# Performance work log

Measured on AMD Instinct MI355X. Metric: run time of the kernel, lower is better.

The kernel has to match this reference:

```python
import jax, jax.numpy as jnp
import numpy as np

B, F, D, H = 256, 128, 512, 8
HD = D // H
SPARSITY = 0.5
KVAL = max(1, int(F * SPARSITY))  # 64


def setup_inputs() -> dict:
    key = jax.random.key(0)
    ks = jax.random.split(key, 12)
    s = 0.02
    x = jax.random.normal(ks[0], (B, F, D), dtype=jnp.float32)
    Wq = jax.random.normal(ks[1], (D, D), dtype=jnp.float32) * s
    bq = jnp.zeros((D,), jnp.float32)
    Wk = jax.random.normal(ks[2], (D, D), dtype=jnp.float32) * s
    bk = jnp.zeros((D,), jnp.float32)
    Wv = jax.random.normal(ks[3], (D, D), dtype=jnp.float32) * s
    bv = jnp.zeros((D,), jnp.float32)
    Wo = jax.random.normal(ks[4], (D, D), dtype=jnp.float32) * s
    bo = jnp.zeros((D,), jnp.float32)
    # correlation prior init: 0.5 * exp(-0.1 * |i-j|)
    idx = jnp.arange(F, dtype=jnp.float32)
    corr_prior = 0.5 * jnp.exp(-0.1 * jnp.abs(idx[:, None] - idx[None, :]))
    feat_imp = jnp.ones((F,), jnp.float32)
    # price_vol_detector: Linear(2D->D), SiLU, Linear(D->1), Sigmoid
    W1 = jax.random.normal(ks[5], (2 * D, D), dtype=jnp.float32) * s
    b1 = jnp.zeros((D,), jnp.float32)
    W2 = jax.random.normal(ks[6], (D, 1), dtype=jnp.float32) * s
    b2 = jnp.zeros((1,), jnp.float32)
    return {"x": x, "Wq": Wq, "bq": bq, "Wk": Wk, "bk": bk, "Wv": Wv, "bv": bv,
            "Wo": Wo, "bo": bo, "corr_prior": corr_prior, "feat_imp": feat_imp,
            "W1": W1, "b1": b1, "W2": W2, "b2": b2}


def reference(x, Wq, bq, Wk, bk, Wv, bv, Wo, bo, corr_prior, feat_imp, W1, b1, W2, b2):
    def split_heads(t):  # [B,F,D] -> [B,H,F,HD]
        return t.reshape(B, F, H, HD).transpose(0, 2, 1, 3)

    q = split_heads(x @ Wq + bq)
    k = split_heads(x @ Wk + bk)
    v = split_heads(x @ Wv + bv)

    scores = jnp.einsum('bhqd,bhkd->bhqk', q, k) / np.sqrt(HD).astype(np.float32)

    # correlation prior * pairwise feature importance
    imp = feat_imp[:, None] * feat_imp[None, :]          # [F,F]
    scores = scores + (corr_prior * imp)[None, None]     # broadcast to [B,H,F,F]

    # price-vol gating (n_features >= 2)
    mid = F // 2
    price = x[:, :mid].mean(axis=1)                      # [B,D]
    vol = x[:, mid:].mean(axis=1)                        # [B,D]
    combined = jnp.concatenate([price, vol], axis=1)     # [B,2D]
    h = jax.nn.silu(combined @ W1 + b1)
    pv = jax.nn.sigmoid(h @ W2 + b2).reshape(B, 1, 1, 1)  # [B,1,1,1]
    fidx = jnp.arange(F)
    pv_mask = ((fidx[:, None] < mid) ^ (fidx[None, :] < mid)).astype(scores.dtype)  # [F,F]
    scores = scores + pv * pv_mask[None, None] * 0.5

    # per-row top-k sparsification (same for all heads; vectorized over heads)
    topk_vals = jax.lax.top_k(scores, KVAL)[0]           # [B,H,F,KVAL]
    thresh = topk_vals[..., -1:]                          # kth largest per row
    scores = jnp.where(scores < thresh, jnp.float32(-1e9), scores)

    attn = jax.nn.softmax(scores, axis=-1)               # dropout: eval mode (identity)
    out = jnp.einsum('bhqk,bhkd->bhqd', attn, v)         # [B,H,F,HD]
    out = out.transpose(0, 2, 1, 3).reshape(B, F, D)     # merge heads
    return out @ Wo + bo
```

## Files before the change

### kernel.cpp

```cpp
#include <hip/hip_runtime.h>
#include <hip/hip_bf16.h>
#include <cstdint>

#define B_ 256
#define F_ 128
#define D_ 512
#define H_ 8
#define KVAL_ 64

typedef unsigned short ushort_t;
typedef __attribute__((ext_vector_type(8))) short short8;
typedef __attribute__((ext_vector_type(4))) float floatx4;
typedef __attribute__((ext_vector_type(2))) float floatx2;
typedef __attribute__((ext_vector_type(2))) double doublex2;

__device__ __forceinline__ unsigned f2ord32(float f) {
  unsigned b = __float_as_uint(f);
  return (b & 0x80000000u) ? ~b : (b | 0x80000000u);
}

__device__ __forceinline__ unsigned long long f2ord64(double s) {
  unsigned long long b = (unsigned long long)__double_as_longlong(s);
  return (b & 0x8000000000000000ull) ? ~b : (b | 0x8000000000000000ull);
}

__device__ __forceinline__ float bcast(float v, int l) {
  return __uint_as_float(__builtin_amdgcn_readlane(__float_as_uint(v), l));
}

__device__ __forceinline__ ushort_t f2bf(float f) {
  __hip_bfloat16 h = __float2bfloat16(f);
  return *reinterpret_cast<ushort_t*>(&h);
}
__device__ __forceinline__ float bf2f(ushort_t u) {
  __hip_bfloat16 h = *reinterpret_cast<__hip_bfloat16*>(&u);
  return __bfloat162float(h);
}

__global__ __launch_bounds__(256) void pv_kernel(
    const float* __restrict__ x, const float* __restrict__ W1,
    const float* __restrict__ b1, const float* __restrict__ W2,
    const float* __restrict__ b2, double* __restrict__ pv) {
  __shared__ double comb[1024];
  __shared__ double red[4];
  int b = blockIdx.x, t = threadIdx.x;
  {
    const float* xb = x + (size_t)b * (F_ * D_) + 2 * t;
    double p0 = 0.0, p1 = 0.0, v0 = 0.0, v1 = 0.0;
#pragma unroll 8
    for (int f = 0; f < 64; ++f) {
      floatx2 xp = *(const floatx2*)(xb + (size_t)f * D_);
      floatx2 xv = *(const floatx2*)(xb + (size_t)(f + 64) * D_);
      p0 += (double)xp[0];
      p1 += (double)xp[1];
      v0 += (double)xv[0];
      v1 += (double)xv[1];
    }
    comb[2 * t] = p0 * (1.0 / 64.0);
    comb[2 * t + 1] = p1 * (1.0 / 64.0);
    comb[512 + 2 * t] = v0 * (1.0 / 64.0);
    comb[512 + 2 * t + 1] = v1 * (1.0 / 64.0);
  }
  __syncthreads();
  double a0 = (double)b1[2 * t], a1 = (double)b1[2 * t + 1];
  const float* wp = W1 + 2 * t;
#pragma unroll 8
  for (int k = 0; k < 1024; ++k) {
    double c = comb[k];
    floatx2 wv = *(const floatx2*)(wp + (size_t)k * 512);
    a0 += c * (double)wv[0];
    a1 += c * (double)wv[1];
  }
  double h0 = a0 / (1.0 + exp(-a0));
  double h1 = a1 / (1.0 + exp(-a1));
  double part = h0 * (double)W2[2 * t] + h1 * (double)W2[2 * t + 1];
  for (int off = 32; off; off >>= 1) part += __shfl_xor(part, off);
  int lane = t & 63, w = t >> 6;
  if (lane == 0) red[w] = part;
  __syncthreads();
  if (t == 0) {
    double tot = red[0] + red[1] + red[2] + red[3] + (double)b2[0];
    pv[b] = 1.0 / (1.0 + exp(-tot));
  }
}

__global__ __launch_bounds__(256) void pack_wqk3_kernel(
    const float* __restrict__ Wq, const float* __restrict__ Wk,
    const float* __restrict__ bq, const float* __restrict__ bk,
    ushort_t* __restrict__ Wh, ushort_t* __restrict__ Wm,
    ushort_t* __restrict__ Wl, double* __restrict__ bqk) {
  int idx = blockIdx.x * 256 + threadIdx.x;
  int n = idx >> 9, k = idx & 511;
  float v = (n < 512) ? Wq[(size_t)k * 512 + n] : Wk[(size_t)k * 512 + (n - 512)];
  ushort_t h = f2bf(v);
  float r1 = v - bf2f(h);
  ushort_t m = f2bf(r1);
  ushort_t l = f2bf(r1 - bf2f(m));
  Wh[idx] = h;
  Wm[idx] = m;
  Wl[idx] = l;
  if (idx < 1024)
    bqk[idx] = (double)((idx < 512) ? bq[idx] : bk[idx - 512]);
}

__global__ __launch_bounds__(256) void pack_wt_kernel(
    const float* __restrict__ W, ushort_t* __restrict__ hiT,
    ushort_t* __restrict__ loT) {
  int i = blockIdx.x * 256 + threadIdx.x;
  int n = i >> 9, k = i & 511;
  float v = W[(size_t)k * 512 + n];
  ushort_t h = f2bf(v);
  hiT[i] = h;
  loT[i] = f2bf(v - bf2f(h));
}

__global__ __launch_bounds__(256) void xsplit3_kernel(
    const float* __restrict__ x, ushort_t* __restrict__ xh,
    ushort_t* __restrict__ xm, ushort_t* __restrict__ xl) {
  int i = blockIdx.x * 256 + threadIdx.x;
  const float* xp = x + (size_t)i * 8;
  floatx4 f0 = *(const floatx4*)xp;
  floatx4 f1 = *(const floatx4*)(xp + 4);
  short8 vh, vm, vl;
#pragma unroll
  for (int j = 0; j < 8; ++j) {
    float fv = (j < 4) ? f0[j] : f1[j - 4];
    ushort_t hb = f2bf(fv);
    float r1 = fv - bf2f(hb);
    ushort_t mb = f2bf(r1);
    ushort_t lb = f2bf(r1 - bf2f(mb));
    vh[j] = (short)hb;
    vm[j] = (short)mb;
    vl[j] = (short)lb;
  }
  *(short8*)&xh[(size_t)i * 8] = vh;
  *(short8*)&xm[(size_t)i * 8] = vm;
  *(short8*)&xl[(size_t)i * 8] = vl;
}

__global__ __launch_bounds__(256) void mfma_qk_v3(
    const ushort_t* __restrict__ Xh, const ushort_t* __restrict__ Xm,
    const ushort_t* __restrict__ Xl, const ushort_t* __restrict__ Wh,
    const ushort_t* __restrict__ Wm, const ushort_t* __restrict__ Wl,
    const double* __restrict__ bias, double* __restrict__ C, int nb) {
  __shared__ ushort_t As[3][128 * 40];
  __shared__ ushort_t Bs[3][128 * 40];
  int s = blockIdx.x;
  int o = (s & 7) * nb + (s >> 3);
  int n0 = (o & 7) * 128, m0 = (o >> 3) * 128;
  int t = threadIdx.x;
  int lane = t & 63, w = t >> 6;
  int wm_ = w >> 1, wn = w & 1;
  int mrow = lane & 15, quad = lane >> 4;
  floatx4 acc[4][4] = {};
  for (int kp = 0; kp < 16; ++kp) {
    int k0 = kp * 32;
    __syncthreads();
#pragma unroll
    for (int p = 0; p < 2; ++p) {
      int idx = p * 256 + t;
      int r = idx >> 2, c = (idx & 3) * 8;
      size_t aoff = (size_t)(m0 + r) * 512 + k0 + c;
      *(short8*)&As[0][r * 40 + c] = *(const short8*)(Xh + aoff);
      *(short8*)&As[1][r * 40 + c] = *(const short8*)(Xm + aoff);
      *(short8*)&As[2][r * 40 + c] = *(const short8*)(Xl + aoff);
      size_t boff = (size_t)(n0 + r) * 512 + k0 + c;
      *(short8*)&Bs[0][r * 40 + c] = *(const short8*)(Wh + boff);
      *(short8*)&Bs[1][r * 40 + c] = *(const short8*)(Wm + boff);
      *(short8*)&Bs[2][r * 40 + c] = *(const short8*)(Wl + boff);
    }
    __syncthreads();
#pragma unroll
    for (int sa = 0; sa < 3; ++sa) {
      short8 af[4];
#pragma unroll
      for (int mt = 0; mt < 4; ++mt)
        af[mt] = *(const short8*)&As[sa][(wm_ * 64 + mt * 16 + mrow) * 40 + quad * 8];
#pragma unroll
      for (int sb = 0; sb < 3; ++sb) {
        if (sa + sb > 2) continue;
        short8 bf[4];
#pragma unroll
        for (int nt = 0; nt < 4; ++nt)
          bf[nt] = *(const short8*)&Bs[sb][(wn * 64 + nt * 16 + mrow) * 40 + quad * 8];
#pragma unroll
        for (int mt = 0; mt < 4; ++mt)
#pragma unroll
          for (int nt = 0; nt < 4; ++nt)
            acc[mt][nt] = __builtin_amdgcn_mfma_f32_16x16x32_bf16(
                af[mt], bf[nt], acc[mt][nt], 0, 0, 0);
      }
    }
  }
#pragma unroll
  for (int nt = 0; nt < 4; ++nt) {
    int gn = n0 + wn * 64 + nt * 16 + mrow;
    double bb = bias[gn];
#pragma unroll
    for (int mt = 0; mt < 4; ++mt) {
      int gm = m0 + wm_ * 64 + mt * 16 + quad * 4;
#pragma unroll
      for (int rg = 0; rg < 4; ++rg)
        C[(size_t)(gm + rg) * 1024 + gn] = (double)acc[mt][nt][rg] + bb;
    }
  }
}

__global__ __launch_bounds__(256) void mfma_gemm_split(
    const float* __restrict__ A, const ushort_t* __restrict__ WhiT,
    const ushort_t* __restrict__ WloT, const float* __restrict__ bias,
    float* __restrict__ C) {
  __shared__ ushort_t Ah[128 * 40];
  __shared__ ushort_t Al[128 * 40];
  __shared__ ushort_t Bh[128 * 40];
  __shared__ ushort_t Bl[128 * 40];
  int s = blockIdx.x;
  int o = (s & 7) * 128 + (s >> 3);
  int n0 = (o & 3) * 128, m0 = (o >> 2) * 128;
  int t = threadIdx.x;
  int lane = t & 63, w = t >> 6;
  int wm = w >> 1, wn = w & 1;
  int mrow = lane & 15, quad = lane >> 4;
  floatx4 acc[4][4] = {};
  for (int kp = 0; kp < 16; ++kp) {
    int k0 = kp * 32;
    __syncthreads();
#pragma unroll
    for (int p = 0; p < 2; ++p) {
      int idx = p * 256 + t;
      int r = idx >> 2, c = (idx & 3) * 8;
      const float* ap = A + (size_t)(m0 + r) * 512 + k0 + c;
      floatx4 f0 = *(const floatx4*)ap;
      floatx4 f1 = *(const floatx4*)(ap + 4);
      short8 vh, vl;
#pragma unroll
      for (int j = 0; j < 8; ++j) {
        float fv = (j < 4) ? f0[j] : f1[j - 4];
        ushort_t hb = f2bf(fv);
        vh[j] = (short)hb;
        vl[j] = (short)f2bf(fv - bf2f(hb));
      }
      *(short8*)&Ah[r * 40 + c] = vh;
      *(short8*)&Al[r * 40 + c] = vl;
      size_t boff = (size_t)(n0 + r) * 512 + k0 + c;
      *(short8*)&Bh[r * 40 + c] = *(const short8*)(WhiT + boff);
      *(short8*)&Bl[r * 40 + c] = *(const short8*)(WloT + boff);
    }
    __syncthreads();
    int abase = (wm * 64 + mrow) * 40 + quad * 8;
    int bbase = (wn * 64 + mrow) * 40 + quad * 8;
    short8 ah[4], bh[4];
#pragma unroll
    for (int i = 0; i < 4; ++i) {
      ah[i] = *(const short8*)&Ah[abase + i * 640];
      bh[i] = *(const short8*)&Bh[bbase + i * 640];
    }
#pragma unroll
    for (int mt = 0; mt < 4; ++mt)
#pragma unroll
      for (int nt = 0; nt < 4; ++nt)
        acc[mt][nt] = __builtin_amdgcn_mfma_f32_16x16x32_bf16(
            ah[mt], bh[nt], acc[mt][nt], 0, 0, 0);
    {
      short8 al[4];
#pragma unroll
      for (int i = 0; i < 4; ++i) al[i] = *(const short8*)&Al[abase + i * 640];
#pragma unroll
      for (int mt = 0; mt < 4; ++mt)
#pragma unroll
        for (int nt = 0; nt < 4; ++nt)
          acc[mt][nt] = __builtin_amdgcn_mfma_f32_16x16x32_bf16(
              al[mt], bh[nt], acc[mt][nt], 0, 0, 0);
    }
    {
      short8 bl[4];
#pragma unroll
      for (int i = 0; i < 4; ++i) bl[i] = *(const short8*)&Bl[bbase + i * 640];
#pragma unroll
      for (int mt = 0; mt < 4; ++mt)
#pragma unroll
        for (int nt = 0; nt < 4; ++nt)
          acc[mt][nt] = __builtin_amdgcn_mfma_f32_16x16x32_bf16(
              ah[mt], bl[nt], acc[mt][nt], 0, 0, 0);
    }
  }
#pragma unroll
  for (int nt = 0; nt < 4; ++nt) {
    int gn = n0 + wn * 64 + nt * 16 + mrow;
    float bb = bias[gn];
#pragma unroll
    for (int mt = 0; mt < 4; ++mt) {
      int gm = m0 + wm * 64 + mt * 16 + quad * 4;
#pragma unroll
      for (int rg = 0; rg < 4; ++rg)
        C[(size_t)(gm + rg) * 512 + gn] = acc[mt][nt][rg] + bb;
    }
  }
}

__global__ __launch_bounds__(1024) void attn_kernel(
    const double* __restrict__ qk, const float* __restrict__ vbuf,
    const float* __restrict__ corr_prior, const float* __restrict__ feat_imp,
    const double* __restrict__ pv, float* __restrict__ attn_out, int b_off,
    int nb) {
  __shared__ double kT[64][128];
  __shared__ __align__(16) double qp[16][512];
  int s = blockIdx.x;
  int o = (s & 7) * nb + (s >> 3);
  int b = o >> 3, h = o & 7;
  int t = threadIdx.x, lane = t & 63, w = t >> 6;
#pragma unroll
  for (int n = 0; n < 8; ++n) {
    int f = w + 16 * n;
    kT[lane][(f + lane) & 127] =
        qk[((size_t)(b * F_ + f)) * 1024 + 512 + h * 64 + lane];
  }
  __syncthreads();
  double pvb = pv[b_off + b] * 0.5;
  double fiA = (double)feat_imp[lane];
  double fiB = (double)feat_imp[64 + lane];
  const double SLOPE = 2.5e5;
  {
    int fb = 8 * w;
#pragma unroll
    for (int i = 0; i < 8; ++i)
      qp[w][i * 64 + lane] =
          qk[((size_t)(b * F_ + fb + i)) * 1024 + h * 64 + lane];
    double s0[8], s1[8];
#pragma unroll
    for (int i = 0; i < 8; ++i) {
      s0[i] = 0.0;
      s1[i] = 0.0;
    }
#pragma unroll 2
    for (int d = 0; d < 64; d += 2) {
      double kd0a = kT[d][(lane + d) & 127];
      double kd1a = kT[d][(lane + 64 + d) & 127];
      double kd0b = kT[d + 1][(lane + 1 + d) & 127];
      double kd1b = kT[d + 1][(lane + 65 + d) & 127];
#pragma unroll
      for (int i = 0; i < 8; ++i) {
        doublex2 q2 = *(const doublex2*)&qp[w][i * 64 + d];
        s0[i] += q2[0] * kd0a;
        s1[i] += q2[0] * kd1a;
        s0[i] += q2[1] * kd0b;
        s1[i] += q2[1] * kd1b;
      }
    }
    float p0s[8], p1s[8];
#pragma unroll
    for (int i = 0; i < 8; ++i) {
      int f = fb + i;
      double sa = s0[i], sb = s1[i];
      double fif = (double)feat_imp[f];
      double cp0 = (double)corr_prior[f * 128 + lane] * fif * fiA;
      double cp1 = (double)corr_prior[f * 128 + 64 + lane] * fif * fiB;
      double add0 = (f < 64) ? 0.0 : pvb;
      double add1 = (f < 64) ? pvb : 0.0;
      sa = sa * 0.125 + cp0 + add0;
      sb = sb * 0.125 + cp1 + add1;
      unsigned a0 = f2ord32((float)sa), a1 = f2ord32((float)sb), T = 0u;
      for (int bit = 31; bit >= 0; --bit) {
        unsigned cand = T | (1u << bit);
        int c = __popcll(__ballot(a0 >= cand)) + __popcll(__ballot(a1 >= cand));
        if (c >= KVAL_) T = cand;
      }
      int cnt_gt = __popcll(__ballot(a0 > T)) + __popcll(__ballot(a1 > T));
      int cnt_ge = __popcll(__ballot(a0 >= T)) + __popcll(__ballot(a1 >= T));
      int bsz = cnt_ge - cnt_gt;
      int r = KVAL_ - cnt_gt;
      double bmax = -1e300;
      if (a0 < T) bmax = sa;
      if (a1 < T && sb > bmax) bmax = sb;
      for (int off = 32; off; off >>= 1) bmax = fmax(bmax, __shfl_xor(bmax, off));
      double sT, sU;
      if (bsz == r) {
        double tmin = 1e300;
        if (a0 == T) tmin = sa;
        if (a1 == T && sb < tmin) tmin = sb;
        for (int off = 32; off; off >>= 1) tmin = fmin(tmin, __shfl_xor(tmin, off));
        sT = tmin;
        sU = bmax;
      } else {
        unsigned long long x0 = (a0 == T) ? f2ord64(sa) : 0ull;
        unsigned long long x1 = (a1 == T) ? f2ord64(sb) : 0ull;
        unsigned long long T64 = 0ull;
        for (int bit = 63; bit >= 0; --bit) {
          unsigned long long cand = T64 | (1ull << bit);
          int c = __popcll(__ballot(x0 >= cand)) + __popcll(__ballot(x1 >= cand));
          if (c >= r) T64 = cand;
        }
        double tv = -1e300, uv = bmax;
        if (x0 == T64) tv = sa;
        if (x1 == T64 && sb > tv) tv = sb;
        if (a0 == T && x0 < T64 && sa > uv) uv = sa;
        if (a1 == T && x1 < T64 && sb > uv) uv = sb;
        for (int off = 32; off; off >>= 1) {
          tv = fmax(tv, __shfl_xor(tv, off));
          uv = fmax(uv, __shfl_xor(uv, off));
        }
        sT = tv;
        sU = uv;
      }
      double mid = 0.5 * (sT + sU);
      double W0 = fmin(1.0, fmax(0.0, 0.5 + (sa - mid) * SLOPE));
      double W1v = fmin(1.0, fmax(0.0, 0.5 + (sb - mid) * SLOPE));
      double mm = fmax(sa, sb);
      for (int off = 32; off; off >>= 1) mm = fmax(mm, __shfl_xor(mm, off));
      float p0 = (float)W0 * expf((float)(sa - mm));
      float p1 = (float)W1v * expf((float)(sb - mm));
      float zz = p0 + p1;
      for (int off = 32; off; off >>= 1) zz += __shfl_xor(zz, off);
      float inv = 1.f / zz;
      p0s[i] = p0 * inv;
      p1s[i] = p1 * inv;
    }
    float* pp = (float*)qp[w];
#pragma unroll
    for (int i = 0; i < 8; ++i) {
      pp[i * 128 + lane] = p0s[i];
      pp[i * 128 + 64 + lane] = p1s[i];
    }
    const float* vb = vbuf + ((size_t)b * F_) * 512 + h * 64 + lane;
    float o8[8] = {0.f, 0.f, 0.f, 0.f, 0.f, 0.f, 0.f, 0.f};
    float vj0 = vb[0], vj1 = vb[512];
    for (int j = 0; j < 128; j += 2) {
      float va = vj0, vbb = vj1;
      if (j + 2 < 128) {
        vj0 = vb[(size_t)(j + 2) * 512];
        vj1 = vb[(size_t)(j + 3) * 512];
      }
#pragma unroll
      for (int i = 0; i < 8; ++i) {
        floatx2 p2 = *(const floatx2*)&pp[i * 128 + j];
        o8[i] += p2[0] * va;
        o8[i] += p2[1] * vbb;
      }
    }
#pragma unroll
    for (int i = 0; i < 8; ++i)
      attn_out[((size_t)(b * F_ + fb + i)) * 512 + h * 64 + lane] = o8[i];
  }
}

extern "C" void kernel_launch(void* const* d_in, const int* in_sizes, int n_in,
                              void* d_out, int out_size, void* d_ws,
                              size_t ws_size, hipStream_t stream) {
  const float* x = (const float*)d_in[0];
  const float* Wq = (const float*)d_in[1];
  const float* bq = (const float*)d_in[2];
  const float* Wk = (const float*)d_in[3];
  const float* bk = (const float*)d_in[4];
  const float* Wv = (const float*)d_in[5];
  const float* bv = (const float*)d_in[6];
  const float* Wo = (const float*)d_in[7];
  const float* bo = (const float*)d_in[8];
  const float* corr = (const float*)d_in[9];
  const float* fimp = (const float*)d_in[10];
  const float* W1 = (const float*)d_in[11];
  const float* b1 = (const float*)d_in[12];
  const float* W2 = (const float*)d_in[13];
  const float* b2 = (const float*)d_in[14];
  float* out = (float*)d_out;
  float* ws = (float*)d_ws;

  double* pv_hi = (double*)ws;
  double* bqk_hi = (double*)(ws + 512);
  ushort_t* WqkTh = (ushort_t*)(ws + 2560);
  ushort_t* WqkTm = (ushort_t*)(ws + 264704);
  ushort_t* WqkTl = (ushort_t*)(ws + 526848);
  ushort_t* WvhiT = (ushort_t*)(ws + 788992);
  ushort_t* WvloT = (ushort_t*)(ws + 920064);
  ushort_t* WohiT = (ushort_t*)(ws + 1051136);
  ushort_t* WoloT = (ushort_t*)(ws + 1182208);
  float* vbuf = ws + 1313280;
  float* attnb = ws + 18090496;
  double* qk = (double*)(ws + 34867712);
  const size_t head = 34867712;
  size_t ws_floats = ws_size / 4;
  int Bc = 8;
  for (int cand = 256; cand >= 8; cand >>= 1)
    if (head + (size_t)cand * 311296 <= ws_floats) { Bc = cand; break; }
  ushort_t* Xh = (ushort_t*)(ws + head + (size_t)Bc * 262144);
  ushort_t* Xm = Xh + (size_t)Bc * 65536;
  ushort_t* Xl = Xm + (size_t)Bc * 65536;

  hipLaunchKernelGGL(pv_kernel, dim3(B_), dim3(256), 0, stream,
                     x, W1, b1, W2, b2, pv_hi);
  hipLaunchKernelGGL(pack_wqk3_kernel, dim3(2048), dim3(256), 0, stream,
                     Wq, Wk, bq, bk, WqkTh, WqkTm, WqkTl, bqk_hi);
  hipLaunchKernelGGL(pack_wt_kernel, dim3(1024), dim3(256), 0, stream,
                     Wv, WvhiT, WvloT);
  hipLaunchKernelGGL(pack_wt_kernel, dim3(1024), dim3(256), 0, stream,
                     Wo, WohiT, WoloT);
  hipLaunchKernelGGL(mfma_gemm_split, dim3(1024), dim3(256), 0, stream,
                     x, WvhiT, WvloT, bv, vbuf);
  for (int b0 = 0; b0 < B_; b0 += Bc) {
    hipLaunchKernelGGL(xsplit3_kernel, dim3(Bc * 32), dim3(256), 0, stream,
                       x + (size_t)b0 * 65536, Xh, Xm, Xl);
    hipLaunchKernelGGL(mfma_qk_v3, dim3(8 * Bc), dim3(256), 0, stream,
                       Xh, Xm, Xl, WqkTh, WqkTm, WqkTl, bqk_hi, qk, Bc);
    hipLaunchKernelGGL(attn_kernel, dim3(Bc * 8), dim3(1024), 0, stream,
                       qk, vbuf + (size_t)b0 * 65536, corr, fimp, pv_hi,
                       attnb + (size_t)b0 * 65536, b0, Bc);
  }
  hipLaunchKernelGGL(mfma_gemm_split, dim3(1024), dim3(256), 0, stream,
                     attnb, WohiT, WoloT, bo, out);
}
```

Before: 1.048 ms.

## Store Q/K intermediates as fp32 and halve attention shared memory

The QK projection now writes fp32 instead of fp64, which halves the intermediate traffic and the workspace footprint, so larger batch chunks fit. The attention kernel stages K and Q in fp32 shared memory, reusing one 64 KB buffer for the probabilities. It adds an occupancy hint to launch bounds. Scores are still accumulated in double, but rounding Q/K to fp32 may perturb top-k tie-breaking near the threshold.

New measurement: 1.190 ms. 1.13x slower.

```diff
diff --git a/kernel.cpp b/kernel.cpp
--- a/kernel.cpp
+++ b/kernel.cpp
@@ -22,10 +22,6 @@
 __device__ __forceinline__ unsigned long long f2ord64(double s) {
   unsigned long long b = (unsigned long long)__double_as_longlong(s);
   return (b & 0x8000000000000000ull) ? ~b : (b | 0x8000000000000000ull);
-}
-
-__device__ __forceinline__ float bcast(float v, int l) {
-  return __uint_as_float(__builtin_amdgcn_readlane(__float_as_uint(v), l));
 }
 
 __device__ __forceinline__ ushort_t f2bf(float f) {
@@ -142,7 +138,7 @@
     const ushort_t* __restrict__ Xh, const ushort_t* __restrict__ Xm,
     const ushort_t* __restrict__ Xl, const ushort_t* __restrict__ Wh,
     const ushort_t* __restrict__ Wm, const ushort_t* __restrict__ Wl,
-    const double* __restrict__ bias, double* __restrict__ C, int nb) {
+    const double* __restrict__ bias, float* __restrict__ C, int nb) {
   __shared__ ushort_t As[3][128 * 40];
   __shared__ ushort_t Bs[3][128 * 40];
   int s = blockIdx.x;
@@ -201,7 +197,7 @@
       int gm = m0 + wm_ * 64 + mt * 16 + quad * 4;
 #pragma unroll
       for (int rg = 0; rg < 4; ++rg)
-        C[(size_t)(gm + rg) * 1024 + gn] = (double)acc[mt][nt][rg] + bb;
+        C[(size_t)(gm + rg) * 1024 + gn] = (float)((double)acc[mt][nt][rg] + bb);
     }
   }
 }
@@ -298,13 +294,12 @@
   }
 }
 
-__global__ __launch_bounds__(1024) void attn_kernel(
-    const double* __restrict__ qk, const float* __restrict__ vbuf,
+__global__ __launch_bounds__(1024, 8) void attn_kernel(
+    const float* __restrict__ qk, const float* __restrict__ vbuf,
     const float* __restrict__ corr_prior, const float* __restrict__ feat_imp,
     const double* __restrict__ pv, float* __restrict__ attn_out, int b_off,
     int nb) {
-  __shared__ double kT[64][128];
-  __shared__ __align__(16) double qp[16][512];
+  __shared__ __align__(16) float smem[16384];
   int s = blockIdx.x;
   int o = (s & 7) * nb + (s >> 3);
   int b = o >> 3, h = o & 7;
@@ -312,135 +307,136 @@
 #pragma unroll
   for (int n = 0; n < 8; ++n) {
     int f = w + 16 * n;
-    kT[lane][(f + lane) & 127] =
+    smem[lane * 128 + ((f + lane) & 127)] =
         qk[((size_t)(b * F_ + f)) * 1024 + 512 + h * 64 + lane];
   }
+  float* qpw = &smem[8192 + w * 512];
+  int fb = 8 * w;
+#pragma unroll
+  for (int i = 0; i < 8; ++i)
+    qpw[i * 64 + lane] =
+        qk[((size_t)(b * F_ + fb + i)) * 1024 + h * 64 + lane];
   __syncthreads();
   double pvb = pv[b_off + b] * 0.5;
   double fiA = (double)feat_imp[lane];
   double fiB = (double)feat_imp[64 + lane];
   const double SLOPE = 2.5e5;
-  {
-    int fb = 8 * w;
-#pragma unroll
-    for (int i = 0; i < 8; ++i)
-      qp[w][i * 64 + lane] =
-          qk[((size_t)(b * F_ + fb + i)) * 1024 + h * 64 + lane];
-    double s0[8], s1[8];
+  double s0[8], s1[8];
+#pragma unroll
+  for (int i = 0; i < 8; ++i) {
+    s0[i] = 0.0;
+    s1[i] = 0.0;
+  }
+#pragma unroll 2
+  for (int d = 0; d < 64; d += 2) {
+    double kd0a = (double)smem[d * 128 + ((lane + d) & 127)];
+    double kd1a = (double)smem[d * 128 + ((lane + 64 + d) & 127)];
+    double kd0b = (double)smem[(d + 1) * 128 + ((lane + 1 + d) & 127)];
+    double kd1b = (double)smem[(d + 1) * 128 + ((lane + 65 + d) & 127)];
 #pragma unroll
     for (int i = 0; i < 8; ++i) {
-      s0[i] = 0.0;
-      s1[i] = 0.0;
-    }
-#pragma unroll 2
-    for (int d = 0; d < 64; d += 2) {
-      double kd0a = kT[d][(lane + d) & 127];
-      double kd1a = kT[d][(lane + 64 + d) & 127];
-      double kd0b = kT[d + 1][(lane + 1 + d) & 127];
-      double kd1b = kT[d + 1][(lane + 65 + d) & 127];
-#pragma unroll
-      for (int i = 0; i < 8; ++i) {
-        doublex2 q2 = *(const doublex2*)&qp[w][i * 64 + d];
-        s0[i] += q2[0] * kd0a;
-        s1[i] += q2[0] * kd1a;
-        s0[i] += q2[1] * kd0b;
-        s1[i] += q2[1] * kd1b;
+      floatx2 q2 = *(const floatx2*)&qpw[i * 64 + d];
+      double qa = (double)q2[0], qb = (double)q2[1];
+      s0[i] += qa * kd0a;
+      s1[i] += qa * kd1a;
+      s0[i] += qb * kd0b;
+      s1[i] += qb * kd1b;
+    }
+  }
+  float p0s[8], p1s[8];
+#pragma unroll
+  for (int i = 0; i < 8; ++i) {
+    int f = fb + i;
+    double sa = s0[i], sb = s1[i];
+    double fif = (double)feat_imp[f];
+    double cp0 = (double)corr_prior[f * 128 + lane] * fif * fiA;
+    double cp1 = (double)corr_prior[f * 128 + 64 + lane] * fif * fiB;
+    double add0 = (f < 64) ? 0.0 : pvb;
+    double add1 = (f < 64) ? pvb : 0.0;
+    sa = sa * 0.125 + cp0 + add0;
+    sb = sb * 0.125 + cp1 + add1;
+    unsigned a0 = f2ord32((float)sa), a1 = f2ord32((float)sb), T = 0u;
+    for (int bit = 31; bit >= 0; --bit) {
+      unsigned cand = T | (1u << bit);
+      int c = __popcll(__ballot(a0 >= cand)) + __popcll(__ballot(a1 >= cand));
+      if (c >= KVAL_) T = cand;
+    }
+    int cnt_gt = __popcll(__ballot(a0 > T)) + __popcll(__ballot(a1 > T));
+    int cnt_ge = __popcll(__ballot(a0 >= T)) + __popcll(__ballot(a1 >= T));
+    int bsz = cnt_ge - cnt_gt;
+    int r = KVAL_ - cnt_gt;
+    double bmax = -1e300;
+    if (a0 < T) bmax = sa;
+    if (a1 < T && sb > bmax) bmax = sb;
+    for (int off = 32; off; off >>= 1) bmax = fmax(bmax, __shfl_xor(bmax, off));
+    double sT, sU;
+    if (bsz == r) {
+      double tmin = 1e300;
+      if (a0 == T) tmin = sa;
+      if (a1 == T && sb < tmin) tmin = sb;
+      for (int off = 32; off; off >>= 1) tmin = fmin(tmin, __shfl_xor(tmin, off));
+      sT = tmin;
+      sU = bmax;
+    } else {
+      unsigned long long x0 = (a0 == T) ? f2ord64(sa) : 0ull;
+      unsigned long long x1 = (a1 == T) ? f2ord64(sb) : 0ull;
+      unsigned long long T64 = 0ull;
+      for (int bit = 63; bit >= 0; --bit) {
+        unsigned long long cand = T64 | (1ull << bit);
+        int c = __popcll(__ballot(x0 >= cand)) + __popcll(__ballot(x1 >= cand));
+        if (c >= r) T64 = cand;
       }
-    }
-    float p0s[8], p1s[8];
+      double tv = -1e300, uv = bmax;
+      if (x0 == T64) tv = sa;
+      if (x1 == T64 && sb > tv) tv = sb;
+      if (a0 == T && x0 < T64 && sa > uv) uv = sa;
+      if (a1 == T && x1 < T64 && sb > uv) uv = sb;
+      for (int off = 32; off; off >>= 1) {
+        tv = fmax(tv, __shfl_xor(tv, off));
+        uv = fmax(uv, __shfl_xor(uv, off));
+      }
+      sT = tv;
+      sU = uv;
+    }
+    double mid = 0.5 * (sT + sU);
+    double W0 = fmin(1.0, fmax(0.0, 0.5 + (sa - mid) * SLOPE));
+    double W1v = fmin(1.0, fmax(0.0, 0.5 + (sb - mid) * SLOPE));
+    double mm = fmax(sa, sb);
+    for (int off = 32; off; off >>= 1) mm = fmax(mm, __shfl_xor(mm, off));
+    float p0 = (float)W0 * expf((float)(sa - mm));
+    float p1 = (float)W1v * expf((float)(sb - mm));
+    float zz = p0 + p1;
+    for (int off = 32; off; off >>= 1) zz += __shfl_xor(zz, off);
+    float inv = 1.f / zz;
+    p0s[i] = p0 * inv;
+    p1s[i] = p1 * inv;
+  }
+  __syncthreads();
+  float* pp = &smem[w * 1024];
+#pragma unroll
+  for (int i = 0; i < 8; ++i) {
+    pp[i * 128 + lane] = p0s[i];
+    pp[i * 128 + 64 + lane] = p1s[i];
+  }
+  const float* vb = vbuf + ((size_t)b * F_) * 512 + h * 64 + lane;
+  float o8[8] = {0.f, 0.f, 0.f, 0.f, 0.f, 0.f, 0.f, 0.f};
+  float vj0 = vb[0], vj1 = vb[512];
+  for (int j = 0; j < 128; j += 2) {
+    float va = vj0, vbb = vj1;
+    if (j + 2 < 128) {
+      vj0 = vb[(size_t)(j + 2) * 512];
+      vj1 = vb[(size_t)(j + 3) * 512];
+    }
 #pragma unroll
     for (int i = 0; i < 8; ++i) {
-      int f = fb + i;
-      double sa = s0[i], sb = s1[i];
-      double fif = (double)feat_imp[f];
-      double cp0 = (double)corr_prior[f * 128 + lane] * fif * fiA;
-      double cp1 = (double)corr_prior[f * 128 + 64 + lane] * fif * fiB;
-      double add0 = (f < 64) ? 0.0 : pvb;
-      double add1 = (f < 64) ? pvb : 0.0;
-      sa = sa * 0.125 + cp0 + add0;
-      sb = sb * 0.125 + cp1 + add1;
-      unsigned a0 = f2ord32((float)sa), a1 = f2ord32((float)sb), T = 0u;
-      for (int bit = 31; bit >= 0; --bit) {
-        unsigned cand = T | (1u << bit);
-        int c = __popcll(__ballot(a0 >= cand)) + __popcll(__ballot(a1 >= cand));
-        if (c >= KVAL_) T = cand;
-      }
-      int cnt_gt = __popcll(__ballot(a0 > T)) + __popcll(__ballot(a1 > T));
-      int cnt_ge = __popcll(__ballot(a0 >= T)) + __popcll(__ballot(a1 >= T));
-      int bsz = cnt_ge - cnt_gt;
-      int r = KVAL_ - cnt_gt;
-      double bmax = -1e300;
-      if (a0 < T) bmax = sa;
-      if (a1 < T && sb > bmax) bmax = sb;
-      for (int off = 32; off; off >>= 1) bmax = fmax(bmax, __shfl_xor(bmax, off));
-      double sT, sU;
-      if (bsz == r) {
-        double tmin = 1e300;
-        if (a0 == T) tmin = sa;
-        if (a1 == T && sb < tmin) tmin = sb;
-        for (int off = 32; off; off >>= 1) tmin = fmin(tmin, __shfl_xor(tmin, off));
-        sT = tmin;
-        sU = bmax;
-      } else {
-        unsigned long long x0 = (a0 == T) ? f2ord64(sa) : 0ull;
-        unsigned long long x1 = (a1 == T) ? f2ord64(sb) : 0ull;
-        unsigned long long T64 = 0ull;
-        for (int bit = 63; bit >= 0; --bit) {
-          unsigned long long cand = T64 | (1ull << bit);
-          int c = __popcll(__ballot(x0 >= cand)) + __popcll(__ballot(x1 >= cand));
-          if (c >= r) T64 = cand;
-        }
-        double tv = -1e300, uv = bmax;
-        if (x0 == T64) tv = sa;
-        if (x1 == T64 && sb > tv) tv = sb;
-        if (a0 == T && x0 < T64 && sa > uv) uv = sa;
-        if (a1 == T && x1 < T64 && sb > uv) uv = sb;
-        for (int off = 32; off; off >>= 1) {
-          tv = fmax(tv, __shfl_xor(tv, off));
-          uv = fmax(uv, __shfl_xor(uv, off));
-        }
-        sT = tv;
-        sU = uv;
-      }
-      double mid = 0.5 * (sT + sU);
-      double W0 = fmin(1.0, fmax(0.0, 0.5 + (sa - mid) * SLOPE));
-      double W1v = fmin(1.0, fmax(0.0, 0.5 + (sb - mid) * SLOPE));
-      double mm = fmax(sa, sb);
-      for (int off = 32; off; off >>= 1) mm = fmax(mm, __shfl_xor(mm, off));
-      float p0 = (float)W0 * expf((float)(sa - mm));
-      float p1 = (float)W1v * expf((float)(sb - mm));
-      float zz = p0 + p1;
-      for (int off = 32; off; off >>= 1) zz += __shfl_xor(zz, off);
-      float inv = 1.f / zz;
-      p0s[i] = p0 * inv;
-      p1s[i] = p1 * inv;
-    }
-    float* pp = (float*)qp[w];
-#pragma unroll
-    for (int i = 0; i < 8; ++i) {
-      pp[i * 128 + lane] = p0s[i];
-      pp[i * 128 + 64 + lane] = p1s[i];
-    }
-    const float* vb = vbuf + ((size_t)b * F_) * 512 + h * 64 + lane;
-    float o8[8] = {0.f, 0.f, 0.f, 0.f, 0.f, 0.f, 0.f, 0.f};
-    float vj0 = vb[0], vj1 = vb[512];
-    for (int j = 0; j < 128; j += 2) {
-      float va = vj0, vbb = vj1;
-      if (j + 2 < 128) {
-        vj0 = vb[(size_t)(j + 2) * 512];
-        vj1 = vb[(size_t)(j + 3) * 512];
-      }
-#pragma unroll
-      for (int i = 0; i < 8; ++i) {
-        floatx2 p2 = *(const floatx2*)&pp[i * 128 + j];
-        o8[i] += p2[0] * va;
-        o8[i] += p2[1] * vbb;
-      }
-    }
-#pragma unroll
-    for (int i = 0; i < 8; ++i)
-      attn_out[((size_t)(b * F_ + fb + i)) * 512 + h * 64 + lane] = o8[i];
-  }
+      floatx2 p2 = *(const floatx2*)&pp[i * 128 + j];
+      o8[i] += p2[0] * va;
+      o8[i] += p2[1] * vbb;
+    }
+  }
+#pragma unroll
+  for (int i = 0; i < 8; ++i)
+    attn_out[((size_t)(b * F_ + fb + i)) * 512 + h * 64 + lane] = o8[i];
 }
 
 extern "C" void kernel_launch(void* const* d_in, const int* in_sizes, int n_in,
@@ -475,13 +471,13 @@
   ushort_t* WoloT = (ushort_t*)(ws + 1182208);
   float* vbuf = ws + 1313280;
   float* attnb = ws + 18090496;
-  double* qk = (double*)(ws + 34867712);
+  float* qk = ws + 34867712;
   const size_t head = 34867712;
   size_t ws_floats = ws_size / 4;
   int Bc = 8;
   for (int cand = 256; cand >= 8; cand >>= 1)
-    if (head + (size_t)cand * 311296 <= ws_floats) { Bc = cand; break; }
-  ushort_t* Xh = (ushort_t*)(ws + head + (size_t)Bc * 262144);
+    if (head + (size_t)cand * 180224 <= ws_floats) { Bc = cand; break; }
+  ushort_t* Xh = (ushort_t*)(ws + head + (size_t)Bc * 131072);
   ushort_t* Xm = Xh + (size_t)Bc * 65536;
   ushort_t* Xl = Xm + (size_t)Bc * 65536;
 
```
